# Kernel tuning notes

Measured on AMD Instinct MI355X. Metric: run time of the kernel, lower is better.

The kernel has to match this reference:

```python
import jax, jax.numpy as jnp
import numpy as np

EMBED_DIM = 256
IDX = 3
SLOT_NORM = True
NEG = -9e15


def setup_inputs() -> dict:
    key = jax.random.key(0)
    ks = jax.random.split(key, 7)
    B, S, D, N = 16, 8192, EMBED_DIM, 64
    return {
        "input_embedding": jax.random.normal(ks[0], (B, S, D), dtype=jnp.float32),
        "mask": jax.random.randint(ks[1], (B, N, S), 0, 2, dtype=jnp.int32),
        "Wv": jax.random.normal(ks[2], (D, D), dtype=jnp.float32) * 0.02,
        "bv": jax.random.normal(ks[3], (D,), dtype=jnp.float32) * 0.02,
        "Wk": jax.random.normal(ks[4], (D, D), dtype=jnp.float32) * 0.02,
        "bk": jax.random.normal(ks[5], (D,), dtype=jnp.float32) * 0.02,
        "queries": jax.random.normal(ks[6], (N, D), dtype=jnp.float32) * 0.02,
    }


def reference(input_embedding, mask, Wv, bv, Wk, bk, queries):
    # values/keys: [B, S, D] (torch Linear: x @ W.T + b)
    values = jnp.einsum("bsd,ed->bse", input_embedding, Wv) + bv
    keys = jnp.einsum("bsd,ed->bse", input_embedding, Wk) + bk
    # attn_logits: [B, N, S]
    logits = jnp.einsum("nd,bsd->bns", queries, keys) / jnp.sqrt(
        jnp.asarray(EMBED_DIM, dtype=keys.dtype)
    )
    logits = jnp.where(mask == 0, jnp.asarray(NEG, dtype=logits.dtype), logits)
    if SLOT_NORM:
        attn = jax.nn.softmax(logits, axis=-2)  # normalize over slots
        attn = attn / jnp.sum(attn, axis=-1, keepdims=True)
    else:
        attn = jax.nn.softmax(logits, axis=-1)
    attention = attn[:, IDX, :][:, None, :]  # [B, 1, S]
    out = jnp.matmul(attention, values)  # [B, 1, D]
    return out, attention
```

## Files before the change

kernel.cpp:

```cpp
#include <hip/hip_runtime.h>


#define B_ 16
#define S_ 8192
#define D_ 256
#define N_ 64
#define LSTR 264

typedef __attribute__((ext_vector_type(8))) short s8_t;
typedef __attribute__((ext_vector_type(4))) float f4_t;
typedef unsigned int u32;
typedef unsigned short u16;

__device__ __forceinline__ u16 f2bf(float f) {
  u32 u = __builtin_bit_cast(u32, f);
  u += 0x7fffu + ((u >> 16) & 1u);
  return (u16)(u >> 16);
}
__device__ __forceinline__ float bflo(u32 p) { return __builtin_bit_cast(float, p << 16); }
__device__ __forceinline__ float bfhi(u32 p) { return __builtin_bit_cast(float, p & 0xffff0000u); }

__global__ void prep_qk(const float* __restrict__ queries, const float* __restrict__ Wk,
                        const float* __restrict__ bk, u16* __restrict__ qf,
                        float* __restrict__ qb) {
  __shared__ float ql[D_];
  __shared__ float rb[D_];
  const int n = blockIdx.x, d = threadIdx.x;
  const float qv = queries[n * D_ + d];
  ql[d] = qv;
  rb[d] = qv * bk[d];
  __syncthreads();
  float a0 = 0.f, a1 = 0.f, a2 = 0.f, a3 = 0.f;
#pragma unroll 4
  for (int e = 0; e < D_; e += 4) {
    a0 = fmaf(ql[e + 0], Wk[(e + 0) * D_ + d], a0);
    a1 = fmaf(ql[e + 1], Wk[(e + 1) * D_ + d], a1);
    a2 = fmaf(ql[e + 2], Wk[(e + 2) * D_ + d], a2);
    a3 = fmaf(ql[e + 3], Wk[(e + 3) * D_ + d], a3);
  }
  const float acc = (a0 + a1) + (a2 + a3);
  const int t4 = n >> 4, c15 = n & 15, c = d >> 5, g = (d >> 3) & 3, j = d & 7;
  qf[((t4 * 8 + c) * 64 + g * 16 + c15) * 8 + j] = f2bf(acc);
  for (int s = 128; s > 0; s >>= 1) { __syncthreads(); if (d < s) rb[d] += rb[d + s]; }
  if (d == 0) qb[n] = rb[0];
}

__global__ __launch_bounds__(256, 2) void attn_main(
    const float* __restrict__ x, const int* __restrict__ mask,
    const u16* __restrict__ qf, const float* __restrict__ qb,
    float* __restrict__ pw, float* __restrict__ dpart, float* __restrict__ att) {
  __shared__ __align__(16) u16 q_lds[16384];
  __shared__ __align__(16) u16 slab[4][16 * LSTR];
  __shared__ u32 pmL[4 * 256];

  const int t = threadIdx.x;
  const int lane = t & 63;
  const int w = t >> 6;
  const int c15 = lane & 15;
  const int g = lane >> 4;
  const int b = blockIdx.y;
  const int sb = blockIdx.x;
  const int s0 = sb * 256;

#pragma unroll
  for (int i = 0; i < 8; ++i)
    ((uint4*)q_lds)[t + 256 * i] = ((const uint4*)qf)[t + 256 * i];

  {
    const int np = t >> 6, s = t & 63;
#pragma unroll
    for (int q = 0; q < 4; ++q) {
      const int* mrow = mask + ((long)b * N_ + np * 16) * S_ + s0 + q * 64 + s;
      u32 bits = 0;
#pragma unroll
      for (int i = 0; i < 16; ++i) bits |= (u32)(mrow[i * S_] != 0) << i;
      pmL[np * 256 + q * 64 + s] = bits;
    }
  }

  const float qbv0 = qb[c15], qbv1 = qb[16 + c15], qbv2 = qb[32 + c15], qbv3 = qb[48 + c15];
  u16* myslab = slab[w];
  const float4* x4 = (const float4*)x;
  const long xbase = ((long)b * S_ + s0 + 16 * w) * 64 + lane;

  f4_t wacc = {0.f, 0.f, 0.f, 0.f};
  float dacc = 0.f;

  float4 pf[16];
#pragma unroll
  for (int r = 0; r < 16; ++r) pf[r] = x4[xbase + (long)r * 64];

  __syncthreads();

#pragma unroll 1
  for (int i = 0; i < 4; ++i) {
#pragma unroll
    for (int r = 0; r < 16; ++r) {
      uint2 h;
      h.x = (u32)f2bf(pf[r].x) | ((u32)f2bf(pf[r].y) << 16);
      h.y = (u32)f2bf(pf[r].z) | ((u32)f2bf(pf[r].w) << 16);
      *(uint2*)&myslab[r * LSTR + lane * 4] = h;
    }
    const long nbase = xbase + (long)((i < 3 ? i + 1 : 3) * 64) * 64;
#pragma unroll
    for (int r = 0; r < 16; ++r) pf[r] = x4[nbase + (long)r * 64];

    const u16* arow = &myslab[c15 * LSTR + g * 8];
    f4_t acc0 = {0.f,0.f,0.f,0.f}, acc1 = {0.f,0.f,0.f,0.f};
    f4_t acc2 = {0.f,0.f,0.f,0.f}, acc3 = {0.f,0.f,0.f,0.f};
#pragma unroll
    for (int c = 0; c < 8; ++c) {
      const s8_t a  = *(const s8_t*)&arow[c * 32];
      acc0 = __builtin_amdgcn_mfma_f32_16x16x32_bf16(a, *(const s8_t*)&q_lds[((0 * 8 + c) * 64 + lane) * 8], acc0, 0, 0, 0);
      acc1 = __builtin_amdgcn_mfma_f32_16x16x32_bf16(a, *(const s8_t*)&q_lds[((1 * 8 + c) * 64 + lane) * 8], acc1, 0, 0, 0);
      acc2 = __builtin_amdgcn_mfma_f32_16x16x32_bf16(a, *(const s8_t*)&q_lds[((2 * 8 + c) * 64 + lane) * 8], acc2, 0, 0, 0);
      acc3 = __builtin_amdgcn_mfma_f32_16x16x32_bf16(a, *(const s8_t*)&q_lds[((3 * 8 + c) * 64 + lane) * 8], acc3, 0, 0, 0);
    }

    float unorm[4];
#pragma unroll
    for (int r = 0; r < 4; ++r) {
      const int sl = i * 64 + 16 * w + g * 4 + r;
      const u32 m0 = pmL[0 * 256 + sl], m1 = pmL[1 * 256 + sl];
      const u32 m2 = pmL[2 * 256 + sl], m3 = pmL[3 * 256 + sl];
      const float e0 = ((m0 >> c15) & 1) ? __expf((acc0[r] + qbv0) * 0.0625f) : 0.f;
      const float e1 = ((m1 >> c15) & 1) ? __expf((acc1[r] + qbv1) * 0.0625f) : 0.f;
      const float e2 = ((m2 >> c15) & 1) ? __expf((acc2[r] + qbv2) * 0.0625f) : 0.f;
      const float e3 = ((m3 >> c15) & 1) ? __expf((acc3[r] + qbv3) * 0.0625f) : 0.f;
      float sm = (e0 + e1) + (e2 + e3);
      sm += __shfl_xor(sm, 1);
      sm += __shfl_xor(sm, 2);
      sm += __shfl_xor(sm, 4);
      sm += __shfl_xor(sm, 8);
      const float en3 = __shfl(e0, (lane & 48) | 3);
      unorm[r] = en3 / sm;
      dacc += unorm[r];
    }
    if (c15 == 3) {
      f4_t u = {unorm[0], unorm[1], unorm[2], unorm[3]};
      *(f4_t*)&att[(long)b * S_ + s0 + i * 64 + 16 * w + g * 4] = u;
    }

#pragma unroll
    for (int r = 0; r < 4; ++r) {
#pragma unroll
      for (int gg = 0; gg < 4; ++gg) {
        const float a_s = __shfl(unorm[r], gg * 16);
        const uint2 h = *(const uint2*)&myslab[(gg * 4 + r) * LSTR + lane * 4];
        wacc[0] = fmaf(a_s, bflo(h.x), wacc[0]);
        wacc[1] = fmaf(a_s, bfhi(h.x), wacc[1]);
        wacc[2] = fmaf(a_s, bflo(h.y), wacc[2]);
        wacc[3] = fmaf(a_s, bfhi(h.y), wacc[3]);
      }
    }
  }

  dacc += __shfl_xor(dacc, 16);
  dacc += __shfl_xor(dacc, 32);

  __syncthreads();
  float* ldsW = (float*)slab;
  if (t < 256) ldsW[t] = 0.f;
  if (t == 0) ldsW[256] = 0.f;
  __syncthreads();
#pragma unroll
  for (int j = 0; j < 4; ++j) atomicAdd(&ldsW[lane * 4 + j], wacc[j]);
  if (lane == 0) atomicAdd(&ldsW[256], dacc);
  __syncthreads();
  const int blk = b * 32 + sb;
  pw[(long)blk * D_ + t] = ldsW[t];
  if (t == 0) dpart[blk] = ldsW[256];
}

__global__ void finalize_k(const float* __restrict__ pw, const float* __restrict__ dpart,
                           const float* __restrict__ Wv, const float* __restrict__ bv,
                           float* __restrict__ out, float* __restrict__ att) {
  __shared__ float red[32];
  __shared__ float wl[D_];
  const int b = blockIdx.x, t = threadIdx.x, part = blockIdx.y;
  if (t < 32) red[t] = dpart[b * 32 + t];
  __syncthreads();
  if (t < 16) red[t] += red[t + 16];
  __syncthreads();
  if (t < 8) red[t] += red[t + 8];
  __syncthreads();
  if (t < 4) red[t] += red[t + 4];
  __syncthreads();
  if (t < 2) red[t] += red[t + 2];
  __syncthreads();
  if (t == 0) red[0] += red[1];
  __syncthreads();
  const float dn = red[0];
  if (part == 0) {
    float s0 = 0.f, s1 = 0.f, s2 = 0.f, s3 = 0.f;
    const float* p = pw + (long)b * 32 * D_ + t;
#pragma unroll 4
    for (int sb = 0; sb < 32; sb += 4) {
      s0 += p[(sb + 0) * D_]; s1 += p[(sb + 1) * D_];
      s2 += p[(sb + 2) * D_]; s3 += p[(sb + 3) * D_];
    }
    wl[t] = (s0 + s1) + (s2 + s3);
    __syncthreads();
    const float4* wr = (const float4*)&Wv[t * D_];
    const float4* wv = (const float4*)wl;
    float d0 = 0.f, d1 = 0.f, d2 = 0.f, d3 = 0.f;
#pragma unroll 8
    for (int e = 0; e < 64; ++e) {
      const float4 a = wv[e], w4 = wr[e];
      d0 = fmaf(a.x, w4.x, d0); d1 = fmaf(a.y, w4.y, d1);
      d2 = fmaf(a.z, w4.z, d2); d3 = fmaf(a.w, w4.w, d3);
    }
    out[b * D_ + t] = ((d0 + d1) + (d2 + d3)) / dn + bv[t];
  } else {
    const float inv = 1.0f / dn;
    att[(long)b * S_ + (part - 1) * 256 + t] *= inv;
  }
}

extern "C" void kernel_launch(void* const* d_in, const int* in_sizes, int n_in,
                              void* d_out, int out_size, void* d_ws, size_t ws_size,
                              hipStream_t stream) {
  const float* x = (const float*)d_in[0];
  const int* mask = (const int*)d_in[1];
  const float* Wv = (const float*)d_in[2];
  const float* bv = (const float*)d_in[3];
  const float* Wk = (const float*)d_in[4];
  const float* bk = (const float*)d_in[5];
  const float* queries = (const float*)d_in[6];

  char* ws = (char*)d_ws;
  u16* qf = (u16*)ws;
  float* qb = (float*)(ws + 32768);
  float* pw = (float*)(ws + 33792);
  float* dpart = (float*)(ws + 33792 + 524288);
  float* out = (float*)d_out;
  float* att = out + B_ * D_;

  prep_qk<<<N_, D_, 0, stream>>>(queries, Wk, bk, qf, qb);
  attn_main<<<dim3(32, B_), 256, 0, stream>>>(x, mask, qf, qb, pw, dpart, att);
  finalize_k<<<dim3(B_, 33), 256, 0, stream>>>(pw, dpart, Wv, bv, out, att);
}
```

Before: 255.9 us.

## Halve per-block sequence chunk, drop LDS query staging and register prefetch

Each attention block now covers 128 sequence positions instead of 256, which doubles the grid to 64x16 blocks and raises the occupancy hint to 4 blocks per CU. The shared-memory copy of the bf16 query fragments is removed and MFMA B-operands are read straight from global (cache-resident) memory. The explicit 16-register software prefetch of x is replaced with direct nontemporal loads, and mask reads are also nontemporal. The aim is more parallelism and less LDS and register pressure to hide HBM latency, at the cost of losing the explicit load/compute overlap and adding more partial sums for finalize to reduce.

Measured after the change: 253.4 us. About the same (-1.0%).

```diff
diff --git a/kernel.cpp b/kernel.cpp
--- a/kernel.cpp
+++ b/kernel.cpp
@@ -45,13 +45,12 @@
   if (d == 0) qb[n] = rb[0];
 }
 
-__global__ __launch_bounds__(256, 2) void attn_main(
+__global__ __launch_bounds__(256, 4) void attn_main(
     const float* __restrict__ x, const int* __restrict__ mask,
     const u16* __restrict__ qf, const float* __restrict__ qb,
     float* __restrict__ pw, float* __restrict__ dpart, float* __restrict__ att) {
-  __shared__ __align__(16) u16 q_lds[16384];
   __shared__ __align__(16) u16 slab[4][16 * LSTR];
-  __shared__ u32 pmL[4 * 256];
+  __shared__ u32 pmL[4 * 128];
 
   const int t = threadIdx.x;
   const int lane = t & 63;
@@ -60,69 +59,60 @@
   const int g = lane >> 4;
   const int b = blockIdx.y;
   const int sb = blockIdx.x;
-  const int s0 = sb * 256;
-
-#pragma unroll
-  for (int i = 0; i < 8; ++i)
-    ((uint4*)q_lds)[t + 256 * i] = ((const uint4*)qf)[t + 256 * i];
+  const int s0 = sb * 128;
 
   {
-    const int np = t >> 6, s = t & 63;
-#pragma unroll
-    for (int q = 0; q < 4; ++q) {
+    const int np = w, s = lane;
+#pragma unroll
+    for (int q = 0; q < 2; ++q) {
       const int* mrow = mask + ((long)b * N_ + np * 16) * S_ + s0 + q * 64 + s;
       u32 bits = 0;
 #pragma unroll
-      for (int i = 0; i < 16; ++i) bits |= (u32)(mrow[i * S_] != 0) << i;
-      pmL[np * 256 + q * 64 + s] = bits;
+      for (int i = 0; i < 16; ++i)
+        bits |= (u32)(__builtin_nontemporal_load(&mrow[i * S_]) != 0) << i;
+      pmL[np * 128 + q * 64 + s] = bits;
     }
   }
 
   const float qbv0 = qb[c15], qbv1 = qb[16 + c15], qbv2 = qb[32 + c15], qbv3 = qb[48 + c15];
   u16* myslab = slab[w];
-  const float4* x4 = (const float4*)x;
-  const long xbase = ((long)b * S_ + s0 + 16 * w) * 64 + lane;
+  const s8_t* qfs = (const s8_t*)qf;
 
   f4_t wacc = {0.f, 0.f, 0.f, 0.f};
   float dacc = 0.f;
 
-  float4 pf[16];
-#pragma unroll
-  for (int r = 0; r < 16; ++r) pf[r] = x4[xbase + (long)r * 64];
-
-  __syncthreads();
-
-#pragma unroll 1
-  for (int i = 0; i < 4; ++i) {
+  __syncthreads();
+
+#pragma unroll
+  for (int i = 0; i < 2; ++i) {
 #pragma unroll
     for (int r = 0; r < 16; ++r) {
+      const f4_t v = __builtin_nontemporal_load(
+          (const f4_t*)&x[(((long)b * S_) + s0 + i * 64 + 16 * w + r) * D_ + lane * 4]);
       uint2 h;
-      h.x = (u32)f2bf(pf[r].x) | ((u32)f2bf(pf[r].y) << 16);
-      h.y = (u32)f2bf(pf[r].z) | ((u32)f2bf(pf[r].w) << 16);
+      h.x = (u32)f2bf(v.x) | ((u32)f2bf(v.y) << 16);
+      h.y = (u32)f2bf(v.z) | ((u32)f2bf(v.w) << 16);
       *(uint2*)&myslab[r * LSTR + lane * 4] = h;
     }
-    const long nbase = xbase + (long)((i < 3 ? i + 1 : 3) * 64) * 64;
-#pragma unroll
-    for (int r = 0; r < 16; ++r) pf[r] = x4[nbase + (long)r * 64];
 
     const u16* arow = &myslab[c15 * LSTR + g * 8];
     f4_t acc0 = {0.f,0.f,0.f,0.f}, acc1 = {0.f,0.f,0.f,0.f};
     f4_t acc2 = {0.f,0.f,0.f,0.f}, acc3 = {0.f,0.f,0.f,0.f};
 #pragma unroll
     for (int c = 0; c < 8; ++c) {
-      const s8_t a  = *(const s8_t*)&arow[c * 32];
-      acc0 = __builtin_amdgcn_mfma_f32_16x16x32_bf16(a, *(const s8_t*)&q_lds[((0 * 8 + c) * 64 + lane) * 8], acc0, 0, 0, 0);
-      acc1 = __builtin_amdgcn_mfma_f32_16x16x32_bf16(a, *(const s8_t*)&q_lds[((1 * 8 + c) * 64 + lane) * 8], acc1, 0, 0, 0);
-      acc2 = __builtin_amdgcn_mfma_f32_16x16x32_bf16(a, *(const s8_t*)&q_lds[((2 * 8 + c) * 64 + lane) * 8], acc2, 0, 0, 0);
-      acc3 = __builtin_amdgcn_mfma_f32_16x16x32_bf16(a, *(const s8_t*)&q_lds[((3 * 8 + c) * 64 + lane) * 8], acc3, 0, 0, 0);
+      const s8_t a = *(const s8_t*)&arow[c * 32];
+      acc0 = __builtin_amdgcn_mfma_f32_16x16x32_bf16(a, qfs[(0 * 8 + c) * 64 + lane], acc0, 0, 0, 0);
+      acc1 = __builtin_amdgcn_mfma_f32_16x16x32_bf16(a, qfs[(1 * 8 + c) * 64 + lane], acc1, 0, 0, 0);
+      acc2 = __builtin_amdgcn_mfma_f32_16x16x32_bf16(a, qfs[(2 * 8 + c) * 64 + lane], acc2, 0, 0, 0);
+      acc3 = __builtin_amdgcn_mfma_f32_16x16x32_bf16(a, qfs[(3 * 8 + c) * 64 + lane], acc3, 0, 0, 0);
     }
 
     float unorm[4];
 #pragma unroll
     for (int r = 0; r < 4; ++r) {
       const int sl = i * 64 + 16 * w + g * 4 + r;
-      const u32 m0 = pmL[0 * 256 + sl], m1 = pmL[1 * 256 + sl];
-      const u32 m2 = pmL[2 * 256 + sl], m3 = pmL[3 * 256 + sl];
+      const u32 m0 = pmL[0 * 128 + sl], m1 = pmL[1 * 128 + sl];
+      const u32 m2 = pmL[2 * 128 + sl], m3 = pmL[3 * 128 + sl];
       const float e0 = ((m0 >> c15) & 1) ? __expf((acc0[r] + qbv0) * 0.0625f) : 0.f;
       const float e1 = ((m1 >> c15) & 1) ? __expf((acc1[r] + qbv1) * 0.0625f) : 0.f;
       const float e2 = ((m2 >> c15) & 1) ? __expf((acc2[r] + qbv2) * 0.0625f) : 0.f;
@@ -167,7 +157,7 @@
   for (int j = 0; j < 4; ++j) atomicAdd(&ldsW[lane * 4 + j], wacc[j]);
   if (lane == 0) atomicAdd(&ldsW[256], dacc);
   __syncthreads();
-  const int blk = b * 32 + sb;
+  const int blk = b * 64 + sb;
   pw[(long)blk * D_ + t] = ldsW[t];
   if (t == 0) dpart[blk] = ldsW[256];
 }
@@ -175,10 +165,12 @@
 __global__ void finalize_k(const float* __restrict__ pw, const float* __restrict__ dpart,
                            const float* __restrict__ Wv, const float* __restrict__ bv,
                            float* __restrict__ out, float* __restrict__ att) {
-  __shared__ float red[32];
+  __shared__ float red[64];
   __shared__ float wl[D_];
   const int b = blockIdx.x, t = threadIdx.x, part = blockIdx.y;
-  if (t < 32) red[t] = dpart[b * 32 + t];
+  if (t < 64) red[t] = dpart[b * 64 + t];
+  __syncthreads();
+  if (t < 32) red[t] += red[t + 32];
   __syncthreads();
   if (t < 16) red[t] += red[t + 16];
   __syncthreads();
@@ -193,9 +185,9 @@
   const float dn = red[0];
   if (part == 0) {
     float s0 = 0.f, s1 = 0.f, s2 = 0.f, s3 = 0.f;
-    const float* p = pw + (long)b * 32 * D_ + t;
+    const float* p = pw + (long)b * 64 * D_ + t;
 #pragma unroll 4
-    for (int sb = 0; sb < 32; sb += 4) {
+    for (int sb = 0; sb < 64; sb += 4) {
       s0 += p[(sb + 0) * D_]; s1 += p[(sb + 1) * D_];
       s2 += p[(sb + 2) * D_]; s3 += p[(sb + 3) * D_];
     }
@@ -232,11 +224,11 @@
   u16* qf = (u16*)ws;
   float* qb = (float*)(ws + 32768);
   float* pw = (float*)(ws + 33792);
-  float* dpart = (float*)(ws + 33792 + 524288);
+  float* dpart = (float*)(ws + 33792 + 1048576);
   float* out = (float*)d_out;
   float* att = out + B_ * D_;
 
   prep_qk<<<N_, D_, 0, stream>>>(queries, Wk, bk, qf, qb);
-  attn_main<<<dim3(32, B_), 256, 0, stream>>>(x, mask, qf, qb, pw, dpart, att);
+  attn_main<<<dim3(64, B_), 256, 0, stream>>>(x, mask, qf, qb, pw, dpart, att);
   finalize_k<<<dim3(B_, 33), 256, 0, stream>>>(pw, dpart, Wv, bv, out, att);
 }
```
